# Kernel optimization log

Hardware: AMD Instinct MI355X
Metric: run time of the kernel (lower is better)

Reference implementation:

```python
import jax, jax.numpy as jnp
import numpy as np

B, H, W, C = 4, 64, 64, 64
DK = C // 8  # key/query channels from Conv2D(filters=channels//8)


def setup_inputs() -> dict:
    key = jax.random.key(0)
    ks = jax.random.split(key, 4)
    x = jax.random.normal(ks[0], (B, H, W, C), dtype=jnp.float32)
    # he_normal-ish scale for 1x1 conv kernels (fan_in = C)
    s = np.sqrt(2.0 / C).astype(np.float32)
    Wf = jax.random.normal(ks[1], (C, DK), dtype=jnp.float32) * s
    Wg = jax.random.normal(ks[2], (C, DK), dtype=jnp.float32) * s
    Wh = jax.random.normal(ks[3], (C, C), dtype=jnp.float32) * s
    bf = jnp.zeros((DK,), dtype=jnp.float32)
    bg = jnp.zeros((DK,), dtype=jnp.float32)
    bh = jnp.zeros((C,), dtype=jnp.float32)
    return {"x": x, "Wf": Wf, "bf": bf, "Wg": Wg, "bg": bg, "Wh": Wh, "bh": bh}


def reference(x, Wf, bf, Wg, bg, Wh, bh):
    b, h, w, c = x.shape
    n = h * w
    xf = x.reshape(b, n, c)  # 1x1 conv == per-position linear over flattened spatial dims
    f = xf @ Wf + bf         # [B, N, DK]
    g = xf @ Wg + bg         # [B, N, DK]
    v = xf @ Wh + bh         # [B, N, C]
    # attention = softmax(g @ f^T) over keys (tf.nn.softmax default: last axis)
    scores = jnp.einsum('bnd,bmd->bnm', g, f)   # [B, N, N]
    attn = jax.nn.softmax(scores, axis=-1)
    out = jnp.einsum('bnm,bmc->bnc', attn, v)   # [B, N, C]
    return out
```

## Files before the change

kernel.cpp:

```cpp
#include <hip/hip_runtime.h>
#include <hip/hip_bf16.h>
#include <hip/hip_fp16.h>

typedef _Float16 half8_t __attribute__((ext_vector_type(8)));
typedef _Float16 half4_t __attribute__((ext_vector_type(4)));
typedef short    short8_t __attribute__((ext_vector_type(8)));
typedef float    f32x4    __attribute__((ext_vector_type(4)));

__global__ __launch_bounds__(256) void prep_kernel(
    const float* __restrict__ x,
    const float* __restrict__ Wf, const float* __restrict__ bf,
    const float* __restrict__ Wg, const float* __restrict__ bg,
    const float* __restrict__ Wh, const float* __restrict__ bh,
    _Float16* __restrict__ fh, _Float16* __restrict__ gh,
    unsigned short* __restrict__ vT)
{
  __shared__ float XsT[64 * 33];
  __shared__ float Wall[64 * 80];
  __shared__ float ball[80];
  const int t  = threadIdx.x;
  const int p0 = blockIdx.x * 32;

  for (int i = t; i < 512; i += 256) {
    Wall[(i >> 3) * 80 + (i & 7)]     = Wf[i];
    Wall[(i >> 3) * 80 + 8 + (i & 7)] = Wg[i];
  }
  for (int i = t; i < 4096; i += 256)
    Wall[(i >> 6) * 80 + 16 + (i & 63)] = Wh[i];
  if (t < 80) ball[t] = (t < 8) ? bf[t] : (t < 16) ? bg[t - 8] : bh[t - 16];

  const float4* xs = (const float4*)(x + (size_t)p0 * 64);
#pragma unroll
  for (int i = 0; i < 2; i++) {
    int idx = t + i * 256;
    int row = idx >> 4, c4 = idx & 15;
    float4 v = xs[idx];
    XsT[(c4 * 4 + 0) * 33 + row] = v.x;
    XsT[(c4 * 4 + 1) * 33 + row] = v.y;
    XsT[(c4 * 4 + 2) * 33 + row] = v.z;
    XsT[(c4 * 4 + 3) * 33 + row] = v.w;
  }
  __syncthreads();

  const int pos = t & 31;
  const int g   = t >> 5;
  const int cb  = g * 10;

  float acc[10];
#pragma unroll
  for (int j = 0; j < 10; j++) acc[j] = ball[cb + j];

  for (int c = 0; c < 64; c++) {
    float xv = XsT[c * 33 + pos];
    const float2* wr = (const float2*)&Wall[c * 80 + cb];
#pragma unroll
    for (int k = 0; k < 5; k++) {
      float2 w2 = wr[k];
      acc[2 * k]     += xv * w2.x;
      acc[2 * k + 1] += xv * w2.y;
    }
  }

  const size_t pg = (size_t)p0 + pos;
  const int b = (int)(pg >> 12);
  const int n = (int)(pg & 4095);
  const size_t vidx = (((size_t)b * 128 + (n >> 5)) * 4 + ((n >> 3) & 3)) * 512 + (n & 7);
#pragma unroll
  for (int j = 0; j < 10; j++) {
    int ch = cb + j;
    if (ch < 8) {
      fh[pg * 8 + ch] = (_Float16)acc[j];
    } else if (ch < 16) {
      gh[pg * 8 + (ch - 8)] = (_Float16)acc[j];
    } else {
      __hip_bfloat16 hv = __float2bfloat16(acc[j]);
      vT[vidx + (size_t)(ch - 16) * 8] = *(unsigned short*)&hv;
    }
  }
}

__device__ __forceinline__ unsigned pack_bf16_2(float lo, float hi) {
  float2 f2; f2.x = lo; f2.y = hi;
  __hip_bfloat162 h2 = __float22bfloat162_rn(f2);
  return *reinterpret_cast<unsigned*>(&h2);
}

__global__ __launch_bounds__(512, 4) void attn_kernel(
    const _Float16* __restrict__ fh,
    const _Float16* __restrict__ gh,
    const unsigned short* __restrict__ vT,
    float* __restrict__ out)
{
  const int N    = 4096;
  const int lane = threadIdx.x & 63;
  const int w    = threadIdx.x >> 6;
  const int quad = lane >> 4;
  const int l15  = lane & 15;

  __shared__ float red[7][64][17];

  const int xcd = blockIdx.x & 7;
  const int b   = xcd >> 1;
  const int sub = ((blockIdx.x >> 3) << 1) + (xcd & 1);
  const int q0  = sub * 16;
  const int kbase = w * 512;

  const _Float16* fbase = fh + (size_t)b * N * 8;
  const _Float16* gbase = gh + (size_t)b * N * 8;
  const short* vbat = (const short*)vT + (size_t)b * 262144 + (quad << 9) + (l15 << 3);

  half8_t gfrag = {};
  if (quad == 0) gfrag = *(const half8_t*)(gbase + (size_t)(q0 + l15) * 8);

  const f32x4 zc = {0.f, 0.f, 0.f, 0.f};
  f32x4 acc[4] = {zc, zc, zc, zc};
  float lpart = 0.f;

  const int  srcA = ((quad & 1) << 5) + l15;
  const int  srcB = srcA + 16;
  const bool hi   = (quad >= 2);

#pragma unroll 8
  for (int cc = 0; cc < 16; cc++) {
    const int k0 = kbase + cc * 32;

    half8_t f0 = {}, f1 = {};
    if (quad == 0) {
      f0 = *(const half8_t*)(fbase + (size_t)(k0 + l15) * 8);
      f1 = *(const half8_t*)(fbase + (size_t)(k0 + 16 + l15) * 8);
    }
    f32x4 s0 = __builtin_amdgcn_mfma_f32_16x16x32_f16(f0, gfrag, zc, 0, 0, 0);
    f32x4 s1 = __builtin_amdgcn_mfma_f32_16x16x32_f16(f1, gfrag, zc, 0, 0, 0);

    float p00 = __expf(s0[0]), p01 = __expf(s0[1]), p02 = __expf(s0[2]), p03 = __expf(s0[3]);
    float p10 = __expf(s1[0]), p11 = __expf(s1[1]), p12 = __expf(s1[2]), p13 = __expf(s1[3]);
    lpart += (p00 + p01 + p02 + p03) + (p10 + p11 + p12 + p13);

    unsigned pk00 = pack_bf16_2(p00, p01), pk01 = pack_bf16_2(p02, p03);
    unsigned pk10 = pack_bf16_2(p10, p11), pk11 = pack_bf16_2(p12, p13);

    unsigned t0aA = __shfl((int)pk00, srcA), t0bA = __shfl((int)pk01, srcA);
    unsigned t1aA = __shfl((int)pk10, srcA), t1bA = __shfl((int)pk11, srcA);
    unsigned t0aB = __shfl((int)pk00, srcB), t0bB = __shfl((int)pk01, srcB);
    unsigned t1aB = __shfl((int)pk10, srcB), t1bB = __shfl((int)pk11, srcB);
    union { unsigned u[4]; short8_t v; } au;
    au.u[0] = hi ? t1aA : t0aA;
    au.u[1] = hi ? t1bA : t0bA;
    au.u[2] = hi ? t1aB : t0aB;
    au.u[3] = hi ? t1bB : t0bB;
    short8_t afrag = au.v;

    const short* vk = vbat + ((size_t)(k0 >> 5) << 11);
    short8_t b0 = *(const short8_t*)(vk);
    short8_t b1 = *(const short8_t*)(vk + 128);
    short8_t b2 = *(const short8_t*)(vk + 256);
    short8_t b3 = *(const short8_t*)(vk + 384);
    acc[0] = __builtin_amdgcn_mfma_f32_16x16x32_bf16(afrag, b0, acc[0], 0, 0, 0);
    acc[1] = __builtin_amdgcn_mfma_f32_16x16x32_bf16(afrag, b1, acc[1], 0, 0, 0);
    acc[2] = __builtin_amdgcn_mfma_f32_16x16x32_bf16(afrag, b2, acc[2], 0, 0, 0);
    acc[3] = __builtin_amdgcn_mfma_f32_16x16x32_bf16(afrag, b3, acc[3], 0, 0, 0);
  }

  float lv = lpart;
  lv += __shfl_xor(lv, 16);
  lv += __shfl_xor(lv, 32);

  if (w > 0) {
    float* p = &red[w - 1][lane][0];
#pragma unroll
    for (int ct = 0; ct < 4; ct++)
#pragma unroll
      for (int reg = 0; reg < 4; reg++) p[ct * 4 + reg] = acc[ct][reg];
    p[16] = lv;
  }
  __syncthreads();
  if (w == 0) {
#pragma unroll
    for (int ww = 0; ww < 7; ww++) {
      const float* p = &red[ww][lane][0];
#pragma unroll
      for (int ct = 0; ct < 4; ct++)
#pragma unroll
        for (int reg = 0; reg < 4; reg++) acc[ct][reg] += p[ct * 4 + reg];
      lv += p[16];
    }
    float inv[4];
#pragma unroll
    for (int reg = 0; reg < 4; reg++)
      inv[reg] = 1.0f / __shfl(lv, quad * 4 + reg);

    float* ob = out + ((size_t)b * N + q0) * 64 + l15;
#pragma unroll
    for (int reg = 0; reg < 4; reg++)
#pragma unroll
      for (int ct = 0; ct < 4; ct++)
        ob[(quad * 4 + reg) * 64 + ct * 16] = acc[ct][reg] * inv[reg];
  }
}

extern "C" void kernel_launch(void* const* d_in, const int* in_sizes, int n_in,
                              void* d_out, int out_size, void* d_ws, size_t ws_size,
                              hipStream_t stream) {
  const float* x  = (const float*)d_in[0];
  const float* Wf = (const float*)d_in[1];
  const float* bf = (const float*)d_in[2];
  const float* Wg = (const float*)d_in[3];
  const float* bg = (const float*)d_in[4];
  const float* Wh = (const float*)d_in[5];
  const float* bh = (const float*)d_in[6];
  float* out = (float*)d_out;

  char* ws = (char*)d_ws;
  _Float16* fh = (_Float16*)ws;
  _Float16* gh = (_Float16*)(ws + 262144);
  unsigned short* vT = (unsigned short*)(ws + 524288);

  prep_kernel<<<512, 256, 0, stream>>>(x, Wf, bf, Wg, bg, Wh, bh, fh, gh, vT);
  attn_kernel<<<1024, 512, 0, stream>>>(fh, gh, vT, out);
}
```

Baseline: 106.2 us.

## Use transposed 16x16x16 bf16 MFMA for PV to drop cross-lane shuffles

When the bf16_1k MFMA builtin is available, the P·V product is computed as V^T·P^T using 16x16x16 bf16 MFMAs. The exp'd score registers then feed the B operand directly, which removes the eight shuffles and selects per iteration. The V workspace layout is reordered to match, and the output store becomes a vectorized float4 per lane with a single reciprocal. It also raises the launch-bounds occupancy hint and lowers the unroll, at the cost of twice as many smaller MFMAs and possible register pressure.

New measurement: 115.7 us. +8.9%, slower.

```diff
diff --git a/kernel.cpp b/kernel.cpp
--- a/kernel.cpp
+++ b/kernel.cpp
@@ -2,9 +2,20 @@
 #include <hip/hip_bf16.h>
 #include <hip/hip_fp16.h>
 
-typedef _Float16 half8_t __attribute__((ext_vector_type(8)));
-typedef _Float16 half4_t __attribute__((ext_vector_type(4)));
+#if defined(__has_builtin)
+#  if __has_builtin(__builtin_amdgcn_mfma_f32_16x16x16bf16_1k)
+#    define USE_BF16_1K 1
+#  else
+#    define USE_BF16_1K 0
+#  endif
+#else
+#  define USE_BF16_1K 0
+#endif
+
+typedef _Float16 half8_t  __attribute__((ext_vector_type(8)));
+typedef _Float16 half4_t  __attribute__((ext_vector_type(4)));
 typedef short    short8_t __attribute__((ext_vector_type(8)));
+typedef short    short4_t __attribute__((ext_vector_type(4)));
 typedef float    f32x4    __attribute__((ext_vector_type(4)));
 
 __global__ __launch_bounds__(256) void prep_kernel(
@@ -64,7 +75,11 @@
   const size_t pg = (size_t)p0 + pos;
   const int b = (int)(pg >> 12);
   const int n = (int)(pg & 4095);
+#if USE_BF16_1K
+  const size_t vidx = ((size_t)b * 256 + (n >> 4)) * 1024 + (n & 15);
+#else
   const size_t vidx = (((size_t)b * 128 + (n >> 5)) * 4 + ((n >> 3) & 3)) * 512 + (n & 7);
+#endif
 #pragma unroll
   for (int j = 0; j < 10; j++) {
     int ch = cb + j;
@@ -74,7 +89,11 @@
       gh[pg * 8 + (ch - 8)] = (_Float16)acc[j];
     } else {
       __hip_bfloat16 hv = __float2bfloat16(acc[j]);
+#if USE_BF16_1K
+      vT[vidx + (size_t)(ch - 16) * 16] = *(unsigned short*)&hv;
+#else
       vT[vidx + (size_t)(ch - 16) * 8] = *(unsigned short*)&hv;
+#endif
     }
   }
 }
@@ -85,7 +104,7 @@
   return *reinterpret_cast<unsigned*>(&h2);
 }
 
-__global__ __launch_bounds__(512, 4) void attn_kernel(
+__global__ __launch_bounds__(512, 6) void attn_kernel(
     const _Float16* __restrict__ fh,
     const _Float16* __restrict__ gh,
     const unsigned short* __restrict__ vT,
@@ -107,7 +126,6 @@
 
   const _Float16* fbase = fh + (size_t)b * N * 8;
   const _Float16* gbase = gh + (size_t)b * N * 8;
-  const short* vbat = (const short*)vT + (size_t)b * 262144 + (quad << 9) + (l15 << 3);
 
   half8_t gfrag = {};
   if (quad == 0) gfrag = *(const half8_t*)(gbase + (size_t)(q0 + l15) * 8);
@@ -116,6 +134,40 @@
   f32x4 acc[4] = {zc, zc, zc, zc};
   float lpart = 0.f;
 
+#if USE_BF16_1K
+  const short* vbat = (const short*)vT + (size_t)b * 262144 + (l15 << 4) + (quad << 2);
+
+#pragma unroll 4
+  for (int cc = 0; cc < 16; cc++) {
+    const int k0 = kbase + cc * 32;
+
+    half8_t f0 = {}, f1 = {};
+    if (quad == 0) {
+      f0 = *(const half8_t*)(fbase + (size_t)(k0 + l15) * 8);
+      f1 = *(const half8_t*)(fbase + (size_t)(k0 + 16 + l15) * 8);
+    }
+    f32x4 s0 = __builtin_amdgcn_mfma_f32_16x16x32_f16(f0, gfrag, zc, 0, 0, 0);
+    f32x4 s1 = __builtin_amdgcn_mfma_f32_16x16x32_f16(f1, gfrag, zc, 0, 0, 0);
+
+    float p00 = __expf(s0[0]), p01 = __expf(s0[1]), p02 = __expf(s0[2]), p03 = __expf(s0[3]);
+    float p10 = __expf(s1[0]), p11 = __expf(s1[1]), p12 = __expf(s1[2]), p13 = __expf(s1[3]);
+    lpart += (p00 + p01 + p02 + p03) + (p10 + p11 + p12 + p13);
+
+    union { unsigned u[2]; short4_t v; } b0u, b1u;
+    b0u.u[0] = pack_bf16_2(p00, p01); b0u.u[1] = pack_bf16_2(p02, p03);
+    b1u.u[0] = pack_bf16_2(p10, p11); b1u.u[1] = pack_bf16_2(p12, p13);
+
+    const short* vk = vbat + ((size_t)(k0 >> 4) << 10);
+#pragma unroll
+    for (int ct = 0; ct < 4; ct++) {
+      short4_t va0 = *(const short4_t*)(vk + ct * 256);
+      short4_t va1 = *(const short4_t*)(vk + 1024 + ct * 256);
+      acc[ct] = __builtin_amdgcn_mfma_f32_16x16x16bf16_1k(va0, b0u.v, acc[ct], 0, 0, 0);
+      acc[ct] = __builtin_amdgcn_mfma_f32_16x16x16bf16_1k(va1, b1u.v, acc[ct], 0, 0, 0);
+    }
+  }
+#else
+  const short* vbat = (const short*)vT + (size_t)b * 262144 + (quad << 9) + (l15 << 3);
   const int  srcA = ((quad & 1) << 5) + l15;
   const int  srcB = srcA + 16;
   const bool hi   = (quad >= 2);
@@ -123,7 +175,6 @@
 #pragma unroll 8
   for (int cc = 0; cc < 16; cc++) {
     const int k0 = kbase + cc * 32;
-
     half8_t f0 = {}, f1 = {};
     if (quad == 0) {
       f0 = *(const half8_t*)(fbase + (size_t)(k0 + l15) * 8);
@@ -160,6 +211,7 @@
     acc[2] = __builtin_amdgcn_mfma_f32_16x16x32_bf16(afrag, b2, acc[2], 0, 0, 0);
     acc[3] = __builtin_amdgcn_mfma_f32_16x16x32_bf16(afrag, b3, acc[3], 0, 0, 0);
   }
+#endif
 
   float lv = lpart;
   lv += __shfl_xor(lv, 16);
@@ -184,17 +236,26 @@
         for (int reg = 0; reg < 4; reg++) acc[ct][reg] += p[ct * 4 + reg];
       lv += p[16];
     }
+#if USE_BF16_1K
+    const float inv = 1.0f / lv;
+    float* ob = out + ((size_t)b * N + q0 + l15) * 64 + (quad << 2);
+#pragma unroll
+    for (int ct = 0; ct < 4; ct++) {
+      f32x4 r = acc[ct] * inv;
+      *(f32x4*)(ob + ct * 16) = r;
+    }
+#else
     float inv[4];
 #pragma unroll
     for (int reg = 0; reg < 4; reg++)
       inv[reg] = 1.0f / __shfl(lv, quad * 4 + reg);
-
     float* ob = out + ((size_t)b * N + q0) * 64 + l15;
 #pragma unroll
     for (int reg = 0; reg < 4; reg++)
 #pragma unroll
       for (int ct = 0; ct < 4; ct++)
         ob[(quad * 4 + reg) * 64 + ct * 16] = acc[ct][reg] * inv[reg];
+#endif
   }
 }
 
```

## Process two query tiles per block and fold log2e into g for exp2

Applied to the files above, without the earlier changes.

Each attention block now handles 32 queries as two 16-query tiles, so every loaded key fragment and V fragment is used twice, and the grid is halved. The g projection weights and bias are pre-scaled by log2(e) in the prep kernel, so the softmax can call the hardware exp2 directly instead of __expf. The cost is higher register pressure from doubled accumulators, an extra LDS reduction round with more barriers, and fewer blocks in flight.

Result: slower. 112.3 us (+5.8%).

```diff
diff --git a/kernel.cpp b/kernel.cpp
--- a/kernel.cpp
+++ b/kernel.cpp
@@ -2,10 +2,11 @@
 #include <hip/hip_bf16.h>
 #include <hip/hip_fp16.h>
 
-typedef _Float16 half8_t __attribute__((ext_vector_type(8)));
-typedef _Float16 half4_t __attribute__((ext_vector_type(4)));
+typedef _Float16 half8_t  __attribute__((ext_vector_type(8)));
 typedef short    short8_t __attribute__((ext_vector_type(8)));
 typedef float    f32x4    __attribute__((ext_vector_type(4)));
+
+#define LOG2E 1.44269504088896f
 
 __global__ __launch_bounds__(256) void prep_kernel(
     const float* __restrict__ x,
@@ -23,11 +24,11 @@
 
   for (int i = t; i < 512; i += 256) {
     Wall[(i >> 3) * 80 + (i & 7)]     = Wf[i];
-    Wall[(i >> 3) * 80 + 8 + (i & 7)] = Wg[i];
+    Wall[(i >> 3) * 80 + 8 + (i & 7)] = Wg[i] * LOG2E;
   }
   for (int i = t; i < 4096; i += 256)
     Wall[(i >> 6) * 80 + 16 + (i & 63)] = Wh[i];
-  if (t < 80) ball[t] = (t < 8) ? bf[t] : (t < 16) ? bg[t - 8] : bh[t - 16];
+  if (t < 80) ball[t] = (t < 8) ? bf[t] : (t < 16) ? bg[t - 8] * LOG2E : bh[t - 16];
 
   const float4* xs = (const float4*)(x + (size_t)p0 * 64);
 #pragma unroll
@@ -102,25 +103,30 @@
   const int xcd = blockIdx.x & 7;
   const int b   = xcd >> 1;
   const int sub = ((blockIdx.x >> 3) << 1) + (xcd & 1);
-  const int q0  = sub * 16;
+  const int qA  = sub * 32;
+  const int qB  = qA + 16;
   const int kbase = w * 512;
 
   const _Float16* fbase = fh + (size_t)b * N * 8;
   const _Float16* gbase = gh + (size_t)b * N * 8;
-  const short* vbat = (const short*)vT + (size_t)b * 262144 + (quad << 9) + (l15 << 3);
-
-  half8_t gfrag = {};
-  if (quad == 0) gfrag = *(const half8_t*)(gbase + (size_t)(q0 + l15) * 8);
+  const short*    vbat  = (const short*)vT + (size_t)b * 262144 + (quad << 9) + (l15 << 3);
+
+  half8_t gfragA = {}, gfragB = {};
+  if (quad == 0) {
+    gfragA = *(const half8_t*)(gbase + (size_t)(qA + l15) * 8);
+    gfragB = *(const half8_t*)(gbase + (size_t)(qB + l15) * 8);
+  }
 
   const f32x4 zc = {0.f, 0.f, 0.f, 0.f};
-  f32x4 acc[4] = {zc, zc, zc, zc};
-  float lpart = 0.f;
+  f32x4 accA[4] = {zc, zc, zc, zc};
+  f32x4 accB[4] = {zc, zc, zc, zc};
+  float lpartA = 0.f, lpartB = 0.f;
 
   const int  srcA = ((quad & 1) << 5) + l15;
   const int  srcB = srcA + 16;
   const bool hi   = (quad >= 2);
 
-#pragma unroll 8
+#pragma unroll 4
   for (int cc = 0; cc < 16; cc++) {
     const int k0 = kbase + cc * 32;
 
@@ -129,49 +135,78 @@
       f0 = *(const half8_t*)(fbase + (size_t)(k0 + l15) * 8);
       f1 = *(const half8_t*)(fbase + (size_t)(k0 + 16 + l15) * 8);
     }
-    f32x4 s0 = __builtin_amdgcn_mfma_f32_16x16x32_f16(f0, gfrag, zc, 0, 0, 0);
-    f32x4 s1 = __builtin_amdgcn_mfma_f32_16x16x32_f16(f1, gfrag, zc, 0, 0, 0);
-
-    float p00 = __expf(s0[0]), p01 = __expf(s0[1]), p02 = __expf(s0[2]), p03 = __expf(s0[3]);
-    float p10 = __expf(s1[0]), p11 = __expf(s1[1]), p12 = __expf(s1[2]), p13 = __expf(s1[3]);
-    lpart += (p00 + p01 + p02 + p03) + (p10 + p11 + p12 + p13);
-
-    unsigned pk00 = pack_bf16_2(p00, p01), pk01 = pack_bf16_2(p02, p03);
-    unsigned pk10 = pack_bf16_2(p10, p11), pk11 = pack_bf16_2(p12, p13);
-
-    unsigned t0aA = __shfl((int)pk00, srcA), t0bA = __shfl((int)pk01, srcA);
-    unsigned t1aA = __shfl((int)pk10, srcA), t1bA = __shfl((int)pk11, srcA);
-    unsigned t0aB = __shfl((int)pk00, srcB), t0bB = __shfl((int)pk01, srcB);
-    unsigned t1aB = __shfl((int)pk10, srcB), t1bB = __shfl((int)pk11, srcB);
-    union { unsigned u[4]; short8_t v; } au;
-    au.u[0] = hi ? t1aA : t0aA;
-    au.u[1] = hi ? t1bA : t0bA;
-    au.u[2] = hi ? t1aB : t0aB;
-    au.u[3] = hi ? t1bB : t0bB;
-    short8_t afrag = au.v;
-
     const short* vk = vbat + ((size_t)(k0 >> 5) << 11);
-    short8_t b0 = *(const short8_t*)(vk);
-    short8_t b1 = *(const short8_t*)(vk + 128);
-    short8_t b2 = *(const short8_t*)(vk + 256);
-    short8_t b3 = *(const short8_t*)(vk + 384);
-    acc[0] = __builtin_amdgcn_mfma_f32_16x16x32_bf16(afrag, b0, acc[0], 0, 0, 0);
-    acc[1] = __builtin_amdgcn_mfma_f32_16x16x32_bf16(afrag, b1, acc[1], 0, 0, 0);
-    acc[2] = __builtin_amdgcn_mfma_f32_16x16x32_bf16(afrag, b2, acc[2], 0, 0, 0);
-    acc[3] = __builtin_amdgcn_mfma_f32_16x16x32_bf16(afrag, b3, acc[3], 0, 0, 0);
-  }
-
-  float lv = lpart;
-  lv += __shfl_xor(lv, 16);
-  lv += __shfl_xor(lv, 32);
+    short8_t v0 = *(const short8_t*)(vk);
+    short8_t v1 = *(const short8_t*)(vk + 128);
+    short8_t v2 = *(const short8_t*)(vk + 256);
+    short8_t v3 = *(const short8_t*)(vk + 384);
+
+    f32x4 s0a = __builtin_amdgcn_mfma_f32_16x16x32_f16(f0, gfragA, zc, 0, 0, 0);
+    f32x4 s1a = __builtin_amdgcn_mfma_f32_16x16x32_f16(f1, gfragA, zc, 0, 0, 0);
+    f32x4 s0b = __builtin_amdgcn_mfma_f32_16x16x32_f16(f0, gfragB, zc, 0, 0, 0);
+    f32x4 s1b = __builtin_amdgcn_mfma_f32_16x16x32_f16(f1, gfragB, zc, 0, 0, 0);
+
+    float pa00 = __builtin_amdgcn_exp2f(s0a[0]), pa01 = __builtin_amdgcn_exp2f(s0a[1]);
+    float pa02 = __builtin_amdgcn_exp2f(s0a[2]), pa03 = __builtin_amdgcn_exp2f(s0a[3]);
+    float pa10 = __builtin_amdgcn_exp2f(s1a[0]), pa11 = __builtin_amdgcn_exp2f(s1a[1]);
+    float pa12 = __builtin_amdgcn_exp2f(s1a[2]), pa13 = __builtin_amdgcn_exp2f(s1a[3]);
+    float pb00 = __builtin_amdgcn_exp2f(s0b[0]), pb01 = __builtin_amdgcn_exp2f(s0b[1]);
+    float pb02 = __builtin_amdgcn_exp2f(s0b[2]), pb03 = __builtin_amdgcn_exp2f(s0b[3]);
+    float pb10 = __builtin_amdgcn_exp2f(s1b[0]), pb11 = __builtin_amdgcn_exp2f(s1b[1]);
+    float pb12 = __builtin_amdgcn_exp2f(s1b[2]), pb13 = __builtin_amdgcn_exp2f(s1b[3]);
+    lpartA += (pa00 + pa01 + pa02 + pa03) + (pa10 + pa11 + pa12 + pa13);
+    lpartB += (pb00 + pb01 + pb02 + pb03) + (pb10 + pb11 + pb12 + pb13);
+
+    {
+      unsigned pk00 = pack_bf16_2(pa00, pa01), pk01 = pack_bf16_2(pa02, pa03);
+      unsigned pk10 = pack_bf16_2(pa10, pa11), pk11 = pack_bf16_2(pa12, pa13);
+      unsigned t0aA = __shfl((int)pk00, srcA), t0bA = __shfl((int)pk01, srcA);
+      unsigned t1aA = __shfl((int)pk10, srcA), t1bA = __shfl((int)pk11, srcA);
+      unsigned t0aB = __shfl((int)pk00, srcB), t0bB = __shfl((int)pk01, srcB);
+      unsigned t1aB = __shfl((int)pk10, srcB), t1bB = __shfl((int)pk11, srcB);
+      union { unsigned u[4]; short8_t v; } au;
+      au.u[0] = hi ? t1aA : t0aA;
+      au.u[1] = hi ? t1bA : t0bA;
+      au.u[2] = hi ? t1aB : t0aB;
+      au.u[3] = hi ? t1bB : t0bB;
+      accA[0] = __builtin_amdgcn_mfma_f32_16x16x32_bf16(au.v, v0, accA[0], 0, 0, 0);
+      accA[1] = __builtin_amdgcn_mfma_f32_16x16x32_bf16(au.v, v1, accA[1], 0, 0, 0);
+      accA[2] = __builtin_amdgcn_mfma_f32_16x16x32_bf16(au.v, v2, accA[2], 0, 0, 0);
+      accA[3] = __builtin_amdgcn_mfma_f32_16x16x32_bf16(au.v, v3, accA[3], 0, 0, 0);
+    }
+    {
+      unsigned pk00 = pack_bf16_2(pb00, pb01), pk01 = pack_bf16_2(pb02, pb03);
+      unsigned pk10 = pack_bf16_2(pb10, pb11), pk11 = pack_bf16_2(pb12, pb13);
+      unsigned t0aA = __shfl((int)pk00, srcA), t0bA = __shfl((int)pk01, srcA);
+      unsigned t1aA = __shfl((int)pk10, srcA), t1bA = __shfl((int)pk11, srcA);
+      unsigned t0aB = __shfl((int)pk00, srcB), t0bB = __shfl((int)pk01, srcB);
+      unsigned t1aB = __shfl((int)pk10, srcB), t1bB = __shfl((int)pk11, srcB);
+      union { unsigned u[4]; short8_t v; } au;
+      au.u[0] = hi ? t1aA : t0aA;
+      au.u[1] = hi ? t1bA : t0bA;
+      au.u[2] = hi ? t1aB : t0aB;
+      au.u[3] = hi ? t1bB : t0bB;
+      accB[0] = __builtin_amdgcn_mfma_f32_16x16x32_bf16(au.v, v0, accB[0], 0, 0, 0);
+      accB[1] = __builtin_amdgcn_mfma_f32_16x16x32_bf16(au.v, v1, accB[1], 0, 0, 0);
+      accB[2] = __builtin_amdgcn_mfma_f32_16x16x32_bf16(au.v, v2, accB[2], 0, 0, 0);
+      accB[3] = __builtin_amdgcn_mfma_f32_16x16x32_bf16(au.v, v3, accB[3], 0, 0, 0);
+    }
+  }
+
+  float lvA = lpartA;
+  lvA += __shfl_xor(lvA, 16);
+  lvA += __shfl_xor(lvA, 32);
+  float lvB = lpartB;
+  lvB += __shfl_xor(lvB, 16);
+  lvB += __shfl_xor(lvB, 32);
 
   if (w > 0) {
     float* p = &red[w - 1][lane][0];
 #pragma unroll
     for (int ct = 0; ct < 4; ct++)
 #pragma unroll
-      for (int reg = 0; reg < 4; reg++) p[ct * 4 + reg] = acc[ct][reg];
-    p[16] = lv;
+      for (int reg = 0; reg < 4; reg++) p[ct * 4 + reg] = accA[ct][reg];
+    p[16] = lvA;
   }
   __syncthreads();
   if (w == 0) {
@@ -181,20 +216,51 @@
 #pragma unroll
       for (int ct = 0; ct < 4; ct++)
 #pragma unroll
-        for (int reg = 0; reg < 4; reg++) acc[ct][reg] += p[ct * 4 + reg];
-      lv += p[16];
+        for (int reg = 0; reg < 4; reg++) accA[ct][reg] += p[ct * 4 + reg];
+      lvA += p[16];
     }
     float inv[4];
 #pragma unroll
     for (int reg = 0; reg < 4; reg++)
-      inv[reg] = 1.0f / __shfl(lv, quad * 4 + reg);
-
-    float* ob = out + ((size_t)b * N + q0) * 64 + l15;
-#pragma unroll
-    for (int reg = 0; reg < 4; reg++)
-#pragma unroll
-      for (int ct = 0; ct < 4; ct++)
-        ob[(quad * 4 + reg) * 64 + ct * 16] = acc[ct][reg] * inv[reg];
+      inv[reg] = 1.0f / __shfl(lvA, quad * 4 + reg);
+    float* ob = out + ((size_t)b * N + qA) * 64 + l15;
+#pragma unroll
+    for (int reg = 0; reg < 4; reg++)
+#pragma unroll
+      for (int ct = 0; ct < 4; ct++)
+        ob[(quad * 4 + reg) * 64 + ct * 16] = accA[ct][reg] * inv[reg];
+  }
+  __syncthreads();
+
+  if (w > 0) {
+    float* p = &red[w - 1][lane][0];
+#pragma unroll
+    for (int ct = 0; ct < 4; ct++)
+#pragma unroll
+      for (int reg = 0; reg < 4; reg++) p[ct * 4 + reg] = accB[ct][reg];
+    p[16] = lvB;
+  }
+  __syncthreads();
+  if (w == 0) {
+#pragma unroll
+    for (int ww = 0; ww < 7; ww++) {
+      const float* p = &red[ww][lane][0];
+#pragma unroll
+      for (int ct = 0; ct < 4; ct++)
+#pragma unroll
+        for (int reg = 0; reg < 4; reg++) accB[ct][reg] += p[ct * 4 + reg];
+      lvB += p[16];
+    }
+    float inv[4];
+#pragma unroll
+    for (int reg = 0; reg < 4; reg++)
+      inv[reg] = 1.0f / __shfl(lvB, quad * 4 + reg);
+    float* ob = out + ((size_t)b * N + qB) * 64 + l15;
+#pragma unroll
+    for (int reg = 0; reg < 4; reg++)
+#pragma unroll
+      for (int ct = 0; ct < 4; ct++)
+        ob[(quad * 4 + reg) * 64 + ct * 16] = accB[ct][reg] * inv[reg];
   }
 }
 
@@ -216,5 +282,5 @@
   unsigned short* vT = (unsigned short*)(ws + 524288);
 
   prep_kernel<<<512, 256, 0, stream>>>(x, Wf, bf, Wg, bg, Wh, bh, fh, gh, vT);
-  attn_kernel<<<1024, 512, 0, stream>>>(fh, gh, vT, out);
-}
+  attn_kernel<<<512, 512, 0, stream>>>(fh, gh, vT, out);
+}
```

## Fold log2e into g weights, use exp2, compute row sums via MFMA

Applied to the files above, without the earlier changes.

Scales the g projection weights and bias by log2(e) in the prep kernel, so the attention kernel can call the hardware exp2 directly instead of __expf. The softmax denominator is now computed by an extra bf16 MFMA of the probability fragment against a vector of ones, replacing the VALU adds and cross-lane shuffles. The V loads are also issued before the score MFMAs to hide latency. The denominator now sums the bf16-rounded probabilities, which matches the numerator, at the cost of one more MFMA per iteration and a larger reduction buffer.

Measured after the change: 105.5 us. No clear change (-0.6%).

```diff
diff --git a/kernel.cpp b/kernel.cpp
--- a/kernel.cpp
+++ b/kernel.cpp
@@ -2,10 +2,11 @@
 #include <hip/hip_bf16.h>
 #include <hip/hip_fp16.h>
 
-typedef _Float16 half8_t __attribute__((ext_vector_type(8)));
-typedef _Float16 half4_t __attribute__((ext_vector_type(4)));
+typedef _Float16 half8_t  __attribute__((ext_vector_type(8)));
 typedef short    short8_t __attribute__((ext_vector_type(8)));
 typedef float    f32x4    __attribute__((ext_vector_type(4)));
+
+#define LOG2E 1.44269504088896f
 
 __global__ __launch_bounds__(256) void prep_kernel(
     const float* __restrict__ x,
@@ -23,11 +24,11 @@
 
   for (int i = t; i < 512; i += 256) {
     Wall[(i >> 3) * 80 + (i & 7)]     = Wf[i];
-    Wall[(i >> 3) * 80 + 8 + (i & 7)] = Wg[i];
+    Wall[(i >> 3) * 80 + 8 + (i & 7)] = Wg[i] * LOG2E;
   }
   for (int i = t; i < 4096; i += 256)
     Wall[(i >> 6) * 80 + 16 + (i & 63)] = Wh[i];
-  if (t < 80) ball[t] = (t < 8) ? bf[t] : (t < 16) ? bg[t - 8] : bh[t - 16];
+  if (t < 80) ball[t] = (t < 8) ? bf[t] : (t < 16) ? bg[t - 8] * LOG2E : bh[t - 16];
 
   const float4* xs = (const float4*)(x + (size_t)p0 * 64);
 #pragma unroll
@@ -97,7 +98,7 @@
   const int quad = lane >> 4;
   const int l15  = lane & 15;
 
-  __shared__ float red[7][64][17];
+  __shared__ float red[7][64][21];
 
   const int xcd = blockIdx.x & 7;
   const int b   = xcd >> 1;
@@ -107,34 +108,46 @@
 
   const _Float16* fbase = fh + (size_t)b * N * 8;
   const _Float16* gbase = gh + (size_t)b * N * 8;
-  const short* vbat = (const short*)vT + (size_t)b * 262144 + (quad << 9) + (l15 << 3);
+  const short*    vbat  = (const short*)vT + (size_t)b * 262144 + (quad << 9) + (l15 << 3);
 
   half8_t gfrag = {};
   if (quad == 0) gfrag = *(const half8_t*)(gbase + (size_t)(q0 + l15) * 8);
 
   const f32x4 zc = {0.f, 0.f, 0.f, 0.f};
   f32x4 acc[4] = {zc, zc, zc, zc};
-  float lpart = 0.f;
+  f32x4 acc4   = zc;
+
+  short8_t ones8;
+#pragma unroll
+  for (int i = 0; i < 8; i++) ones8[i] = (short)0x3F80;
 
   const int  srcA = ((quad & 1) << 5) + l15;
   const int  srcB = srcA + 16;
   const bool hi   = (quad >= 2);
 
+  half8_t f0 = {}, f1 = {};
+
 #pragma unroll 8
   for (int cc = 0; cc < 16; cc++) {
     const int k0 = kbase + cc * 32;
 
-    half8_t f0 = {}, f1 = {};
     if (quad == 0) {
       f0 = *(const half8_t*)(fbase + (size_t)(k0 + l15) * 8);
       f1 = *(const half8_t*)(fbase + (size_t)(k0 + 16 + l15) * 8);
     }
+    const short* vk = vbat + ((size_t)(k0 >> 5) << 11);
+    short8_t v0 = *(const short8_t*)(vk);
+    short8_t v1 = *(const short8_t*)(vk + 128);
+    short8_t v2 = *(const short8_t*)(vk + 256);
+    short8_t v3 = *(const short8_t*)(vk + 384);
+
     f32x4 s0 = __builtin_amdgcn_mfma_f32_16x16x32_f16(f0, gfrag, zc, 0, 0, 0);
     f32x4 s1 = __builtin_amdgcn_mfma_f32_16x16x32_f16(f1, gfrag, zc, 0, 0, 0);
 
-    float p00 = __expf(s0[0]), p01 = __expf(s0[1]), p02 = __expf(s0[2]), p03 = __expf(s0[3]);
-    float p10 = __expf(s1[0]), p11 = __expf(s1[1]), p12 = __expf(s1[2]), p13 = __expf(s1[3]);
-    lpart += (p00 + p01 + p02 + p03) + (p10 + p11 + p12 + p13);
+    float p00 = __builtin_amdgcn_exp2f(s0[0]), p01 = __builtin_amdgcn_exp2f(s0[1]);
+    float p02 = __builtin_amdgcn_exp2f(s0[2]), p03 = __builtin_amdgcn_exp2f(s0[3]);
+    float p10 = __builtin_amdgcn_exp2f(s1[0]), p11 = __builtin_amdgcn_exp2f(s1[1]);
+    float p12 = __builtin_amdgcn_exp2f(s1[2]), p13 = __builtin_amdgcn_exp2f(s1[3]);
 
     unsigned pk00 = pack_bf16_2(p00, p01), pk01 = pack_bf16_2(p02, p03);
     unsigned pk10 = pack_bf16_2(p10, p11), pk11 = pack_bf16_2(p12, p13);
@@ -150,20 +163,12 @@
     au.u[3] = hi ? t1bB : t0bB;
     short8_t afrag = au.v;
 
-    const short* vk = vbat + ((size_t)(k0 >> 5) << 11);
-    short8_t b0 = *(const short8_t*)(vk);
-    short8_t b1 = *(const short8_t*)(vk + 128);
-    short8_t b2 = *(const short8_t*)(vk + 256);
-    short8_t b3 = *(const short8_t*)(vk + 384);
-    acc[0] = __builtin_amdgcn_mfma_f32_16x16x32_bf16(afrag, b0, acc[0], 0, 0, 0);
-    acc[1] = __builtin_amdgcn_mfma_f32_16x16x32_bf16(afrag, b1, acc[1], 0, 0, 0);
-    acc[2] = __builtin_amdgcn_mfma_f32_16x16x32_bf16(afrag, b2, acc[2], 0, 0, 0);
-    acc[3] = __builtin_amdgcn_mfma_f32_16x16x32_bf16(afrag, b3, acc[3], 0, 0, 0);
-  }
-
-  float lv = lpart;
-  lv += __shfl_xor(lv, 16);
-  lv += __shfl_xor(lv, 32);
+    acc[0] = __builtin_amdgcn_mfma_f32_16x16x32_bf16(afrag, v0, acc[0], 0, 0, 0);
+    acc[1] = __builtin_amdgcn_mfma_f32_16x16x32_bf16(afrag, v1, acc[1], 0, 0, 0);
+    acc[2] = __builtin_amdgcn_mfma_f32_16x16x32_bf16(afrag, v2, acc[2], 0, 0, 0);
+    acc[3] = __builtin_amdgcn_mfma_f32_16x16x32_bf16(afrag, v3, acc[3], 0, 0, 0);
+    acc4   = __builtin_amdgcn_mfma_f32_16x16x32_bf16(afrag, ones8, acc4, 0, 0, 0);
+  }
 
   if (w > 0) {
     float* p = &red[w - 1][lane][0];
@@ -171,7 +176,8 @@
     for (int ct = 0; ct < 4; ct++)
 #pragma unroll
       for (int reg = 0; reg < 4; reg++) p[ct * 4 + reg] = acc[ct][reg];
-    p[16] = lv;
+#pragma unroll
+    for (int reg = 0; reg < 4; reg++) p[16 + reg] = acc4[reg];
   }
   __syncthreads();
   if (w == 0) {
@@ -182,12 +188,12 @@
       for (int ct = 0; ct < 4; ct++)
 #pragma unroll
         for (int reg = 0; reg < 4; reg++) acc[ct][reg] += p[ct * 4 + reg];
-      lv += p[16];
+#pragma unroll
+      for (int reg = 0; reg < 4; reg++) acc4[reg] += p[16 + reg];
     }
     float inv[4];
 #pragma unroll
-    for (int reg = 0; reg < 4; reg++)
-      inv[reg] = 1.0f / __shfl(lv, quad * 4 + reg);
+    for (int reg = 0; reg < 4; reg++) inv[reg] = 1.0f / acc4[reg];
 
     float* ob = out + ((size_t)b * N + q0) * 64 + l15;
 #pragma unroll
```
